# Kernel optimization log

Hardware: AMD Instinct MI355X
Metric: run time of the kernel (lower is better)

Reference implementation:

```python
import jax, jax.numpy as jnp
import numpy as np

N_NODES = 50000
N_EDGES = 1250000
IN_CH = 64
HID = 64
N_CLASSES = 10
N_GRAPHS = 128


def _xavier(key, shape):
    fan_out, fan_in = shape
    limit = np.sqrt(6.0 / (fan_in + fan_out))
    return jax.random.uniform(key, shape, jnp.float32, -limit, limit)


def setup_inputs() -> dict:
    key = jax.random.key(0)
    ks = jax.random.split(key, 12)
    x = jax.random.normal(ks[0], (N_NODES, IN_CH), jnp.float32)
    edge_index = jax.random.randint(ks[1], (2, N_EDGES), 0, N_NODES, jnp.int64)
    batch = jnp.sort(jax.random.randint(ks[2], (N_NODES,), 0, N_GRAPHS, jnp.int64))
    return {
        "x": x,
        "edge_index": edge_index,
        "batch": batch,
        # GraphConv i: lin_rel (weight+bias) applied to aggregated neighbors,
        # lin_root (no bias) applied to self features. Weights are [out, in].
        "W1_rel": _xavier(ks[3], (HID, IN_CH)), "b1": jnp.zeros((HID,), jnp.float32),
        "W1_root": _xavier(ks[4], (HID, IN_CH)),
        "W2_rel": _xavier(ks[5], (HID, HID)), "b2": jnp.zeros((HID,), jnp.float32),
        "W2_root": _xavier(ks[6], (HID, HID)),
        "W3_rel": _xavier(ks[7], (HID, HID)), "b3": jnp.zeros((HID,), jnp.float32),
        "W3_root": _xavier(ks[8], (HID, HID)),
        "W_lin": _xavier(ks[9], (N_CLASSES, HID)), "b_lin": jnp.zeros((N_CLASSES,), jnp.float32),
    }


def _graph_conv(x, src, dst, W_rel, b, W_root):
    # sum-aggregate neighbor features: gather at src, scatter-add at dst
    agg = jax.ops.segment_sum(x[src], dst, num_segments=N_NODES)  # [N, F]
    return agg @ W_rel.T + b + x @ W_root.T


def reference(x, edge_index, batch, W1_rel, b1, W1_root, W2_rel, b2, W2_root,
              W3_rel, b3, W3_root, W_lin, b_lin):
    src, dst = edge_index[0], edge_index[1]
    h = jax.nn.relu(_graph_conv(x, src, dst, W1_rel, b1, W1_root))
    h = jax.nn.relu(_graph_conv(h, src, dst, W2_rel, b2, W2_root))
    h = _graph_conv(h, src, dst, W3_rel, b3, W3_root)
    # global mean pool over graphs
    sums = jax.ops.segment_sum(h, batch, num_segments=N_GRAPHS)        # [G, HID]
    counts = jax.ops.segment_sum(jnp.ones((h.shape[0],), h.dtype), batch,
                                 num_segments=N_GRAPHS)
    pooled = sums / jnp.maximum(counts, 1.0)[:, None]
    out = pooled @ W_lin.T + b_lin  # dropout inactive in eval mode
    return (pooled, out)
```

## Files before the change

kernel.cpp:

```cpp
#include <hip/hip_runtime.h>

#define N_NODES   50000
#define HID       64
#define N_GRAPHS  128
#define N_CLASSES 10
#define NP        196
#define EPA       8192
#define PCAP      8192

typedef __attribute__((ext_vector_type(8))) short short8;
typedef __attribute__((ext_vector_type(4))) float f32x4;

__device__ __forceinline__ unsigned bf16rne(float f) {
    unsigned u = __float_as_uint(f);
    return (u + 0x7fffu + ((u >> 16) & 1u)) >> 16;
}
__device__ __forceinline__ unsigned pack_bf16x2(float lo, float hi) {
    return bf16rne(lo) | (bf16rne(hi) << 16);
}



__global__ void cvt_kernel(const float* __restrict__ x, unsigned short* __restrict__ xb,
                           int* __restrict__ gcursor, const int* __restrict__ batch,
                           int* __restrict__ gstart) {
    int i = blockIdx.x * blockDim.x + threadIdx.x;
    if (blockIdx.x == 0 && threadIdx.x < NP) gcursor[threadIdx.x] = 0;
    if (i < N_NODES) {
        int b = batch[i];
        int bp = (i > 0) ? batch[i - 1] : -1;
        for (int g = bp + 1; g <= b; ++g) gstart[g] = i;
        if (i == N_NODES - 1)
            for (int g = b + 1; g <= N_GRAPHS; ++g) gstart[g] = N_NODES;
    }
    if (i < N_NODES * 16) {
        float4 v = ((const float4*)x)[i];
        uint2 o;
        o.x = pack_bf16x2(v.x, v.y);
        o.y = pack_bf16x2(v.z, v.w);
        ((uint2*)xb)[i] = o;
    }
}


__global__ __launch_bounds__(256) void bucket_kernel(
    const int* __restrict__ src, const int* __restrict__ dst,
    int* __restrict__ gcursor, unsigned* __restrict__ packed, int E) {
    __shared__ int hist[NP], scp[NP], base[NP], cnt2[NP];
    __shared__ int sc[256];
    __shared__ unsigned stag[EPA];
    const int t = threadIdx.x;
    const int e0 = blockIdx.x * EPA;
    const int e1 = min(e0 + EPA, E);
    for (int i = t; i < NP; i += 256) { hist[i] = 0; cnt2[i] = 0; }
    __syncthreads();
    for (int e = e0 + t; e < e1; e += 256)
        atomicAdd(&hist[dst[e] >> 8], 1);
    __syncthreads();
    sc[t] = (t < NP) ? hist[t] : 0;
    __syncthreads();
    for (int off = 1; off < 256; off <<= 1) {
        int add = (t >= off) ? sc[t - off] : 0;
        __syncthreads();
        sc[t] += add;
        __syncthreads();
    }
    if (t < NP) {
        scp[t] = sc[t] - hist[t];
        if (hist[t] > 0) base[t] = atomicAdd(&gcursor[t], hist[t]);
    }
    __syncthreads();
    for (int e = e0 + t; e < e1; e += 256) {
        int d = dst[e], s = src[e];
        int p = d >> 8;
        int idx = scp[p] + atomicAdd(&cnt2[p], 1);
        stag[idx] = (unsigned)s | ((unsigned)(d & 255) << 16) | ((unsigned)p << 24);
    }
    __syncthreads();
    const int n = e1 - e0;
    for (int i = t; i < n; i += 256) {
        unsigned v = stag[i];
        int p = v >> 24;
        packed[(size_t)p * PCAP + base[p] + (i - scp[p])] = v & 0x00FFFFFFu;
    }
}

__global__ __launch_bounds__(256) void build_kernel(
    const unsigned* __restrict__ packed, const int* __restrict__ gcursor,
    int* __restrict__ offsets, unsigned short* __restrict__ csr,
    int* __restrict__ sums_zero) {
    __shared__ int hist[256], lofs[256], cnt[256], sc[256], gv[256];
    __shared__ unsigned short lcsr[PCAP];
    const int p = blockIdx.x, t = threadIdx.x;

    if (p == 0) {
        for (int i = t; i < N_GRAPHS * 64; i += 256) sums_zero[i] = 0;
    }

    int v = (t < NP) ? gcursor[t] : 0;
    sc[t] = v; gv[t] = v;
    __syncthreads();
    for (int off = 1; off < 256; off <<= 1) {
        int add = (t >= off) ? sc[t - off] : 0;
        __syncthreads();
        sc[t] += add;
        __syncthreads();
    }
    const int pb = sc[p] - gv[p];
    const int ne = gv[p];
    if (p == NP - 1 && t == 0) offsets[N_NODES] = sc[NP - 1];
    __syncthreads();

    const unsigned* mypk = packed + (size_t)p * PCAP;
    hist[t] = 0; cnt[t] = 0;
    __syncthreads();
    for (int i = t; i < ne; i += 256)
        atomicAdd(&hist[(mypk[i] >> 16) & 255], 1);
    __syncthreads();
    sc[t] = hist[t];
    __syncthreads();
    for (int off = 1; off < 256; off <<= 1) {
        int add = (t >= off) ? sc[t - off] : 0;
        __syncthreads();
        sc[t] += add;
        __syncthreads();
    }
    lofs[t] = sc[t] - hist[t];
    int node = p * 256 + t;
    if (node < N_NODES) offsets[node] = pb + lofs[t];
    __syncthreads();
    for (int i = t; i < ne; i += 256) {
        unsigned vv = mypk[i];
        int dl = (vv >> 16) & 255;
        int slot = lofs[dl] + atomicAdd(&cnt[dl], 1);
        lcsr[slot] = (unsigned short)(vv & 0xFFFFu);
    }
    __syncthreads();
    for (int i = t; i < ne; i += 256) csr[pb + i] = lcsr[i];
}


template <int RELU, int POOL>
__global__ __launch_bounds__(256) void layer_kernel(
    const unsigned short* __restrict__ hin,
    const int* __restrict__ offsets, const unsigned short* __restrict__ csr_src,
    const float* __restrict__ Wrel, const float* __restrict__ bias,
    const float* __restrict__ Wroot, unsigned short* __restrict__ hout,
    const int* __restrict__ batch, float* __restrict__ sums) {
    __shared__ short8 wfrag[2][4][2][4][16];
    __shared__ unsigned short agg_lds[32][72];

    const int tid = threadIdx.x;
    const int w = tid >> 6, lane = tid & 63;
    const int g0 = blockIdx.x * 32;

    for (int f = tid; f < 1024; f += 256) {
        int m = f >> 9;
        int r = f & 511;
        int t = r >> 7, s = (r >> 6) & 1, q = (r >> 4) & 3, c = r & 15;
        const float* W = m ? Wroot : Wrel;
        const float4* pw = (const float4*)(W + (t * 16 + c) * 64 + s * 32 + q * 8);
        float4 v0 = pw[0], v1 = pw[1];
        short8 fr;
        fr[0] = (short)bf16rne(v0.x); fr[1] = (short)bf16rne(v0.y);
        fr[2] = (short)bf16rne(v0.z); fr[3] = (short)bf16rne(v0.w);
        fr[4] = (short)bf16rne(v1.x); fr[5] = (short)bf16rne(v1.y);
        fr[6] = (short)bf16rne(v1.z); fr[7] = (short)bf16rne(v1.w);
        wfrag[m][t][s][q][c] = fr;
    }

    {
        const int rg = lane >> 3;
        const int cg = lane & 7;
        const int nb = g0 + w * 8;
        int myoff = (lane < 9) ? offsets[min(nb + lane, N_NODES)] : 0;
        for (int i = 0; i < 8; ++i) {
            const int beg = __shfl(myoff, i), end = __shfl(myoff, i + 1);
            float acc[8] = {0.f, 0.f, 0.f, 0.f, 0.f, 0.f, 0.f, 0.f};
            for (int base = beg; base < end; base += 64) {
                int cnt = min(64, end - base);
                int sidx = (base + lane < end) ? (int)csr_src[base + lane] : 0;
                for (int kb = 0; kb < cnt; kb += 32) {
                    uint4 u[4];
#pragma unroll
                    for (int p = 0; p < 4; ++p) {
                        int e = kb + 8 * p + rg;
                        int r = __shfl(sidx, e);
                        u[p] = (e < cnt) ? *((const uint4*)(hin + (size_t)r * 64) + cg)
                                         : make_uint4(0u, 0u, 0u, 0u);
                    }
#pragma unroll
                    for (int p = 0; p < 4; ++p) {
                        acc[0] += __uint_as_float(u[p].x << 16);
                        acc[1] += __uint_as_float(u[p].x & 0xffff0000u);
                        acc[2] += __uint_as_float(u[p].y << 16);
                        acc[3] += __uint_as_float(u[p].y & 0xffff0000u);
                        acc[4] += __uint_as_float(u[p].z << 16);
                        acc[5] += __uint_as_float(u[p].z & 0xffff0000u);
                        acc[6] += __uint_as_float(u[p].w << 16);
                        acc[7] += __uint_as_float(u[p].w & 0xffff0000u);
                    }
                }
            }
#pragma unroll
            for (int m = 8; m <= 32; m <<= 1)
#pragma unroll
                for (int j = 0; j < 8; ++j)
                    acc[j] += __shfl_xor(acc[j], m);
            if (rg == 0) {
                uint4 o;
                o.x = pack_bf16x2(acc[0], acc[1]);
                o.y = pack_bf16x2(acc[2], acc[3]);
                o.z = pack_bf16x2(acc[4], acc[5]);
                o.w = pack_bf16x2(acc[6], acc[7]);
                *((uint4*)&agg_lds[w * 8 + i][cg * 8]) = o;
            }
        }
    }

    __syncthreads();

    const int ng = w >> 1;
    const int th = w & 1;
    const int q = lane >> 4, c = lane & 15;
    const int n0 = g0 + ng * 16;

    short8 a_agg[2], a_x[2];
#pragma unroll
    for (int s = 0; s < 2; ++s) {
        a_agg[s] = *(const short8*)&agg_lds[ng * 16 + c][s * 32 + q * 8];
        a_x[s]   = *(const short8*)(hin + (size_t)min(n0 + c, N_NODES - 1) * 64 + s * 32 + q * 8);
    }

    f32x4 acc4[2];
#pragma unroll
    for (int tt = 0; tt < 2; ++tt) {
        const int t = th * 2 + tt;
        float bv = bias[t * 16 + c];
        f32x4 a0 = {bv, bv, bv, bv};
        a0 = __builtin_amdgcn_mfma_f32_16x16x32_bf16(a_agg[0], wfrag[0][t][0][q][c], a0, 0, 0, 0);
        a0 = __builtin_amdgcn_mfma_f32_16x16x32_bf16(a_agg[1], wfrag[0][t][1][q][c], a0, 0, 0, 0);
        a0 = __builtin_amdgcn_mfma_f32_16x16x32_bf16(a_x[0],   wfrag[1][t][0][q][c], a0, 0, 0, 0);
        a0 = __builtin_amdgcn_mfma_f32_16x16x32_bf16(a_x[1],   wfrag[1][t][1][q][c], a0, 0, 0, 0);
        acc4[tt] = a0;
    }

    if (POOL) {
        int nlast = n0 + 15;
        int b0 = batch[min(n0, N_NODES - 1)];
        int b15 = (nlast < N_NODES) ? batch[nlast] : -1;
        if (b0 == b15) {
#pragma unroll
            for (int tt = 0; tt < 2; ++tt) {
                const int t = th * 2 + tt;
                float s = acc4[tt][0] + acc4[tt][1] + acc4[tt][2] + acc4[tt][3];
                s += __shfl_xor(s, 16);
                s += __shfl_xor(s, 32);
                if (q == 0) atomicAdd(&sums[b0 * 64 + t * 16 + c], s);
            }
        } else {
#pragma unroll
            for (int r = 0; r < 4; ++r) {
                int n = n0 + q * 4 + r;
                if (n < N_NODES) {
                    int bq = batch[n];
#pragma unroll
                    for (int tt = 0; tt < 2; ++tt)
                        atomicAdd(&sums[bq * 64 + (th * 2 + tt) * 16 + c], acc4[tt][r]);
                }
            }
        }
    } else {
        __syncthreads();
#pragma unroll
        for (int tt = 0; tt < 2; ++tt) {
            const int t = th * 2 + tt;
#pragma unroll
            for (int r = 0; r < 4; ++r) {
                float v = acc4[tt][r];
                if (RELU) v = fmaxf(v, 0.f);
                agg_lds[ng * 16 + q * 4 + r][t * 16 + c] = (unsigned short)bf16rne(v);
            }
        }
        __syncthreads();
        {
            int row = w * 8 + (lane >> 3);
            int ch = (lane & 7) * 8;
            int n = g0 + row;
            if (n < N_NODES) {
                short8 v = *(const short8*)&agg_lds[row][ch];
                *(short8*)(hout + (size_t)n * 64 + ch) = v;
            }
        }
    }
}


__global__ void final_kernel(const float* __restrict__ sums, const int* __restrict__ gstart,
                             const float* __restrict__ Wlin, const float* __restrict__ blin,
                             float* __restrict__ out) {
    __shared__ float pl[64];
    int g = blockIdx.x, lane = threadIdx.x;
    float cdiv = fmaxf((float)(gstart[g + 1] - gstart[g]), 1.0f);
    float p = sums[g * 64 + lane] / cdiv;
    out[g * 64 + lane] = p;
    pl[lane] = p;
    __syncthreads();
    if (lane < N_CLASSES) {
        float o = blin[lane];
#pragma unroll
        for (int k = 0; k < 64; ++k) o += pl[k] * Wlin[lane * 64 + k];
        out[N_GRAPHS * 64 + g * N_CLASSES + lane] = o;
    }
}


extern "C" void kernel_launch(void* const* d_in, const int* in_sizes, int n_in,
                              void* d_out, int out_size, void* d_ws, size_t ws_size,
                              hipStream_t stream) {
    const float* x     = (const float*)d_in[0];
    const int*   ei    = (const int*)d_in[1];
    const int*   batch = (const int*)d_in[2];
    const float* W1r = (const float*)d_in[3];
    const float* b1  = (const float*)d_in[4];
    const float* W1o = (const float*)d_in[5];
    const float* W2r = (const float*)d_in[6];
    const float* b2  = (const float*)d_in[7];
    const float* W2o = (const float*)d_in[8];
    const float* W3r = (const float*)d_in[9];
    const float* b3  = (const float*)d_in[10];
    const float* W3o = (const float*)d_in[11];
    const float* Wl  = (const float*)d_in[12];
    const float* bl  = (const float*)d_in[13];
    float* out = (float*)d_out;

    const int E = in_sizes[1] / 2;
    const int* src = ei;
    const int* dst = ei + E;

    char* p = (char*)d_ws;
    unsigned short* xb  = (unsigned short*)p; p += (size_t)N_NODES * 64 * 2;
    unsigned short* h1  = (unsigned short*)p; p += (size_t)N_NODES * 64 * 2;
    unsigned short* h2  = (unsigned short*)p; p += (size_t)N_NODES * 64 * 2;
    unsigned* packed    = (unsigned*)p; p += (size_t)NP * PCAP * 4;
    unsigned short* csr = (unsigned short*)p; p += (size_t)E * 2;
    int* offsets   = (int*)p;   p += (size_t)(N_NODES + 1) * 4;
    int* gcursor   = (int*)p;   p += NP * 4;
    float* sums    = (float*)p; p += (size_t)N_GRAPHS * 64 * 4;
    int* gstart    = (int*)p;   p += (N_GRAPHS + 1) * 4;

    const int NCHUNK = (E + EPA - 1) / EPA;
    cvt_kernel<<<(N_NODES * 16 + 255) / 256, 256, 0, stream>>>(x, xb, gcursor, batch, gstart);
    bucket_kernel<<<NCHUNK, 256, 0, stream>>>(src, dst, gcursor, packed, E);
    build_kernel<<<NP, 256, 0, stream>>>(packed, gcursor, offsets, csr, (int*)sums);

    const int LB = (N_NODES + 31) / 32;
    layer_kernel<1, 0><<<LB, 256, 0, stream>>>(xb, offsets, csr, W1r, b1, W1o, h1, batch, sums);
    layer_kernel<1, 0><<<LB, 256, 0, stream>>>(h1, offsets, csr, W2r, b2, W2o, h2, batch, sums);
    layer_kernel<0, 1><<<LB, 256, 0, stream>>>(h2, offsets, csr, W3r, b3, W3o, h1, batch, sums);

    final_kernel<<<N_GRAPHS, 64, 0, stream>>>(sums, gstart, Wl, bl, out);
}
```

Baseline: 234.2 us.

## Split node features into two channel-half planes and gather each half separately

Node features in bf16 are now stored as two planes of 32 channels each (64 bytes per node) in place of one interleaved 128-byte row. The aggregation gathers neighbours one plane at a time, with 8-byte loads per lane and half as many accumulators. The aim is to shrink the working set of each gather pass so it fits better in cache, and to cut register pressure. The cost is walking the edge list twice and issuing twice as many smaller, less efficient gather loads.

```diff
diff --git a/kernel.cpp b/kernel.cpp
--- a/kernel.cpp
+++ b/kernel.cpp
@@ -7,6 +7,7 @@
 #define NP        196
 #define EPA       8192
 #define PCAP      8192
+#define NS32      ((size_t)N_NODES * 32)
 
 typedef __attribute__((ext_vector_type(8))) short short8;
 typedef __attribute__((ext_vector_type(4))) float f32x4;
@@ -38,7 +39,9 @@
         uint2 o;
         o.x = pack_bf16x2(v.x, v.y);
         o.y = pack_bf16x2(v.z, v.w);
-        ((uint2*)xb)[i] = o;
+        int node = i >> 4, grp = i & 15;
+        int s = grp >> 3;
+        *((uint2*)(xb + (size_t)s * NS32 + (size_t)node * 32) + (grp & 7)) = o;
     }
 }
 
@@ -174,46 +177,44 @@
         const int cg = lane & 7;
         const int nb = g0 + w * 8;
         int myoff = (lane < 9) ? offsets[min(nb + lane, N_NODES)] : 0;
-        for (int i = 0; i < 8; ++i) {
-            const int beg = __shfl(myoff, i), end = __shfl(myoff, i + 1);
-            float acc[8] = {0.f, 0.f, 0.f, 0.f, 0.f, 0.f, 0.f, 0.f};
-            for (int base = beg; base < end; base += 64) {
-                int cnt = min(64, end - base);
-                int sidx = (base + lane < end) ? (int)csr_src[base + lane] : 0;
-                for (int kb = 0; kb < cnt; kb += 32) {
-                    uint4 u[4];
-#pragma unroll
-                    for (int p = 0; p < 4; ++p) {
-                        int e = kb + 8 * p + rg;
-                        int r = __shfl(sidx, e);
-                        u[p] = (e < cnt) ? *((const uint4*)(hin + (size_t)r * 64) + cg)
-                                         : make_uint4(0u, 0u, 0u, 0u);
-                    }
-#pragma unroll
-                    for (int p = 0; p < 4; ++p) {
-                        acc[0] += __uint_as_float(u[p].x << 16);
-                        acc[1] += __uint_as_float(u[p].x & 0xffff0000u);
-                        acc[2] += __uint_as_float(u[p].y << 16);
-                        acc[3] += __uint_as_float(u[p].y & 0xffff0000u);
-                        acc[4] += __uint_as_float(u[p].z << 16);
-                        acc[5] += __uint_as_float(u[p].z & 0xffff0000u);
-                        acc[6] += __uint_as_float(u[p].w << 16);
-                        acc[7] += __uint_as_float(u[p].w & 0xffff0000u);
+#pragma unroll
+        for (int sl = 0; sl < 2; ++sl) {
+            const unsigned short* hsl = hin + (size_t)sl * NS32;
+            for (int i = 0; i < 8; ++i) {
+                const int beg = __shfl(myoff, i), end = __shfl(myoff, i + 1);
+                float acc[4] = {0.f, 0.f, 0.f, 0.f};
+                for (int base = beg; base < end; base += 64) {
+                    int cnt = min(64, end - base);
+                    int sidx = (base + lane < end) ? (int)csr_src[base + lane] : 0;
+                    for (int kb = 0; kb < cnt; kb += 32) {
+                        uint2 u[4];
+#pragma unroll
+                        for (int p = 0; p < 4; ++p) {
+                            int e = kb + 8 * p + rg;
+                            int r = __shfl(sidx, e);
+                            u[p] = (e < cnt) ? *((const uint2*)(hsl + (size_t)r * 32) + cg)
+                                             : make_uint2(0u, 0u);
+                        }
+#pragma unroll
+                        for (int p = 0; p < 4; ++p) {
+                            acc[0] += __uint_as_float(u[p].x << 16);
+                            acc[1] += __uint_as_float(u[p].x & 0xffff0000u);
+                            acc[2] += __uint_as_float(u[p].y << 16);
+                            acc[3] += __uint_as_float(u[p].y & 0xffff0000u);
+                        }
                     }
                 }
-            }
-#pragma unroll
-            for (int m = 8; m <= 32; m <<= 1)
-#pragma unroll
-                for (int j = 0; j < 8; ++j)
-                    acc[j] += __shfl_xor(acc[j], m);
-            if (rg == 0) {
-                uint4 o;
-                o.x = pack_bf16x2(acc[0], acc[1]);
-                o.y = pack_bf16x2(acc[2], acc[3]);
-                o.z = pack_bf16x2(acc[4], acc[5]);
-                o.w = pack_bf16x2(acc[6], acc[7]);
-                *((uint4*)&agg_lds[w * 8 + i][cg * 8]) = o;
+#pragma unroll
+                for (int m = 8; m <= 32; m <<= 1)
+#pragma unroll
+                    for (int j = 0; j < 4; ++j)
+                        acc[j] += __shfl_xor(acc[j], m);
+                if (rg == 0) {
+                    uint2 o;
+                    o.x = pack_bf16x2(acc[0], acc[1]);
+                    o.y = pack_bf16x2(acc[2], acc[3]);
+                    *((uint2*)&agg_lds[w * 8 + i][sl * 32 + cg * 4]) = o;
+                }
             }
         }
     }
@@ -229,7 +230,8 @@
 #pragma unroll
     for (int s = 0; s < 2; ++s) {
         a_agg[s] = *(const short8*)&agg_lds[ng * 16 + c][s * 32 + q * 8];
-        a_x[s]   = *(const short8*)(hin + (size_t)min(n0 + c, N_NODES - 1) * 64 + s * 32 + q * 8);
+        a_x[s]   = *(const short8*)(hin + (size_t)s * NS32
+                       + (size_t)min(n0 + c, N_NODES - 1) * 32 + q * 8);
     }
 
     f32x4 acc4[2];
@@ -286,10 +288,11 @@
         {
             int row = w * 8 + (lane >> 3);
             int ch = (lane & 7) * 8;
+            int s = ch >> 5;
             int n = g0 + row;
             if (n < N_NODES) {
                 short8 v = *(const short8*)&agg_lds[row][ch];
-                *(short8*)(hout + (size_t)n * 64 + ch) = v;
+                *(short8*)(hout + (size_t)s * NS32 + (size_t)n * 32 + (ch & 31)) = v;
             }
         }
     }
```

Result: slower. 251.4 us (+7.3%).

## Software-pipeline neighbor gathers across nodes with double-buffered loads; halve EPA

Applied to the files above, without the earlier changes.

Restructures the per-warp neighbor aggregation so that all eight nodes' CSR indices are loaded up front. The first 32-edge gather for the next node is issued before the current node is consumed, using two alternating register buffers. This aims to hide global gather latency behind the accumulate and reduction work, at the cost of more registers and possibly lower occupancy. It also halves the EPA constant, which changes a work-partition size in another phase.

```diff
diff --git a/kernel.cpp b/kernel.cpp
--- a/kernel.cpp
+++ b/kernel.cpp
@@ -5,7 +5,7 @@
 #define N_GRAPHS  128
 #define N_CLASSES 10
 #define NP        196
-#define EPA       8192
+#define EPA       4096
 #define PCAP      8192
 
 typedef __attribute__((ext_vector_type(8))) short short8;
@@ -174,48 +174,102 @@
         const int cg = lane & 7;
         const int nb = g0 + w * 8;
         int myoff = (lane < 9) ? offsets[min(nb + lane, N_NODES)] : 0;
+        int begs[8], cnts[8], sidx[8];
+#pragma unroll
         for (int i = 0; i < 8; ++i) {
-            const int beg = __shfl(myoff, i), end = __shfl(myoff, i + 1);
-            float acc[8] = {0.f, 0.f, 0.f, 0.f, 0.f, 0.f, 0.f, 0.f};
-            for (int base = beg; base < end; base += 64) {
-                int cnt = min(64, end - base);
-                int sidx = (base + lane < end) ? (int)csr_src[base + lane] : 0;
-                for (int kb = 0; kb < cnt; kb += 32) {
-                    uint4 u[4];
-#pragma unroll
-                    for (int p = 0; p < 4; ++p) {
-                        int e = kb + 8 * p + rg;
-                        int r = __shfl(sidx, e);
-                        u[p] = (e < cnt) ? *((const uint4*)(hin + (size_t)r * 64) + cg)
-                                         : make_uint4(0u, 0u, 0u, 0u);
-                    }
-#pragma unroll
-                    for (int p = 0; p < 4; ++p) {
-                        acc[0] += __uint_as_float(u[p].x << 16);
-                        acc[1] += __uint_as_float(u[p].x & 0xffff0000u);
-                        acc[2] += __uint_as_float(u[p].y << 16);
-                        acc[3] += __uint_as_float(u[p].y & 0xffff0000u);
-                        acc[4] += __uint_as_float(u[p].z << 16);
-                        acc[5] += __uint_as_float(u[p].z & 0xffff0000u);
-                        acc[6] += __uint_as_float(u[p].w << 16);
-                        acc[7] += __uint_as_float(u[p].w & 0xffff0000u);
-                    }
-                }
-            }
-#pragma unroll
-            for (int m = 8; m <= 32; m <<= 1)
-#pragma unroll
-                for (int j = 0; j < 8; ++j)
-                    acc[j] += __shfl_xor(acc[j], m);
-            if (rg == 0) {
-                uint4 o;
-                o.x = pack_bf16x2(acc[0], acc[1]);
-                o.y = pack_bf16x2(acc[2], acc[3]);
-                o.z = pack_bf16x2(acc[4], acc[5]);
-                o.w = pack_bf16x2(acc[6], acc[7]);
-                *((uint4*)&agg_lds[w * 8 + i][cg * 8]) = o;
-            }
-        }
+            int beg = __shfl(myoff, i), end = __shfl(myoff, i + 1);
+            begs[i] = beg; cnts[i] = end - beg;
+            sidx[i] = (beg + lane < end) ? (int)csr_src[beg + lane] : 0;
+        }
+
+        uint4 bA[4], bB[4];
+#define LOADN(i, buf)                                                         \
+        {                                                                     \
+            _Pragma("unroll")                                                 \
+            for (int p = 0; p < 4; ++p) {                                     \
+                int e = 8 * p + rg;                                           \
+                int r = __shfl(sidx[i], e);                                   \
+                buf[p] = (e < cnts[i])                                        \
+                    ? *((const uint4*)(hin + (size_t)r * 64) + cg)            \
+                    : make_uint4(0u, 0u, 0u, 0u);                             \
+            }                                                                 \
+        }
+#define UNPACK(buf, acc)                                                      \
+        {                                                                     \
+            _Pragma("unroll")                                                 \
+            for (int p = 0; p < 4; ++p) {                                     \
+                acc[0] += __uint_as_float(buf[p].x << 16);                    \
+                acc[1] += __uint_as_float(buf[p].x & 0xffff0000u);            \
+                acc[2] += __uint_as_float(buf[p].y << 16);                    \
+                acc[3] += __uint_as_float(buf[p].y & 0xffff0000u);            \
+                acc[4] += __uint_as_float(buf[p].z << 16);                    \
+                acc[5] += __uint_as_float(buf[p].z & 0xffff0000u);            \
+                acc[6] += __uint_as_float(buf[p].w << 16);                    \
+                acc[7] += __uint_as_float(buf[p].w & 0xffff0000u);            \
+            }                                                                 \
+        }
+#define CONSUME(i, buf)                                                       \
+        {                                                                     \
+            float acc[8] = {0.f,0.f,0.f,0.f,0.f,0.f,0.f,0.f};                 \
+            UNPACK(buf, acc);                                                 \
+            if (cnts[i] > 32) {               \
+                uint4 u2[4];                                                  \
+                _Pragma("unroll")                                             \
+                for (int p = 0; p < 4; ++p) {                                 \
+                    int e = 32 + 8 * p + rg;                                  \
+                    int r = __shfl(sidx[i], e);                               \
+                    u2[p] = (e < cnts[i])                                     \
+                        ? *((const uint4*)(hin + (size_t)r * 64) + cg)        \
+                        : make_uint4(0u, 0u, 0u, 0u);                         \
+                }                                                             \
+                UNPACK(u2, acc);                                              \
+            }                                                                 \
+            if (cnts[i] > 64) {                 \
+                int end = begs[i] + cnts[i];                                  \
+                for (int base = begs[i] + 64; base < end; base += 64) {       \
+                    int cnt = min(64, end - base);                            \
+                    int sid = (base + lane < end) ? (int)csr_src[base + lane] : 0; \
+                    for (int kb = 0; kb < cnt; kb += 32) {                    \
+                        uint4 u3[4];                                          \
+                        _Pragma("unroll")                                     \
+                        for (int p = 0; p < 4; ++p) {                         \
+                            int e = kb + 8 * p + rg;                          \
+                            int r = __shfl(sid, e);                           \
+                            u3[p] = (e < cnt)                                 \
+                                ? *((const uint4*)(hin + (size_t)r * 64) + cg) \
+                                : make_uint4(0u, 0u, 0u, 0u);                 \
+                        }                                                     \
+                        UNPACK(u3, acc);                                      \
+                    }                                                         \
+                }                                                             \
+            }                                                                 \
+            _Pragma("unroll")                                                 \
+            for (int m = 8; m <= 32; m <<= 1)                                 \
+                _Pragma("unroll")                                             \
+                for (int j = 0; j < 8; ++j)                                   \
+                    acc[j] += __shfl_xor(acc[j], m);                          \
+            if (rg == 0) {                                                    \
+                uint4 o;                                                      \
+                o.x = pack_bf16x2(acc[0], acc[1]);                            \
+                o.y = pack_bf16x2(acc[2], acc[3]);                            \
+                o.z = pack_bf16x2(acc[4], acc[5]);                            \
+                o.w = pack_bf16x2(acc[6], acc[7]);                            \
+                *((uint4*)&agg_lds[w * 8 + (i)][cg * 8]) = o;                 \
+            }                                                                 \
+        }
+
+        LOADN(0, bA); LOADN(1, bB);
+        CONSUME(0, bA); LOADN(2, bA);
+        CONSUME(1, bB); LOADN(3, bB);
+        CONSUME(2, bA); LOADN(4, bA);
+        CONSUME(3, bB); LOADN(5, bB);
+        CONSUME(4, bA); LOADN(6, bA);
+        CONSUME(5, bB); LOADN(7, bB);
+        CONSUME(6, bA);
+        CONSUME(7, bB);
+#undef LOADN
+#undef UNPACK
+#undef CONSUME
     }
 
     __syncthreads();
```

Result: no change. 234.8 us (+0.2%).

## Fuse all stages into one cooperative persistent kernel with grid syncs

Applied to the files above, without the earlier changes.

Replaces the seven separate launches (convert, bucket, build, three layers, final) with a single cooperative persistent kernel. Work is distributed over virtual blocks in grid-stride loops, and grid.sync() separates the stages. The intent is to remove per-launch overhead and the inter-kernel gaps, and the edge chunk size is halved to raise parallelism in the bucket phase. The cost is grid-wide barriers, a capped resident grid that may lower occupancy in the layer phases, and a non-inlined layer function.

```diff
diff --git a/kernel.cpp b/kernel.cpp
--- a/kernel.cpp
+++ b/kernel.cpp
@@ -1,12 +1,17 @@
 #include <hip/hip_runtime.h>
+#include <hip/hip_cooperative_groups.h>
+
+namespace cg = cooperative_groups;
 
 #define N_NODES   50000
 #define HID       64
 #define N_GRAPHS  128
 #define N_CLASSES 10
 #define NP        196
-#define EPA       8192
+#define EPA       4096
 #define PCAP      8192
+#define NCVT      3125
+#define NVL       1563
 
 typedef __attribute__((ext_vector_type(8))) short short8;
 typedef __attribute__((ext_vector_type(4))) float f32x4;
@@ -19,144 +24,29 @@
     return bf16rne(lo) | (bf16rne(hi) << 16);
 }
 
-
-
-__global__ void cvt_kernel(const float* __restrict__ x, unsigned short* __restrict__ xb,
-                           int* __restrict__ gcursor, const int* __restrict__ batch,
-                           int* __restrict__ gstart) {
-    int i = blockIdx.x * blockDim.x + threadIdx.x;
-    if (blockIdx.x == 0 && threadIdx.x < NP) gcursor[threadIdx.x] = 0;
-    if (i < N_NODES) {
-        int b = batch[i];
-        int bp = (i > 0) ? batch[i - 1] : -1;
-        for (int g = bp + 1; g <= b; ++g) gstart[g] = i;
-        if (i == N_NODES - 1)
-            for (int g = b + 1; g <= N_GRAPHS; ++g) gstart[g] = N_NODES;
-    }
-    if (i < N_NODES * 16) {
-        float4 v = ((const float4*)x)[i];
-        uint2 o;
-        o.x = pack_bf16x2(v.x, v.y);
-        o.y = pack_bf16x2(v.z, v.w);
-        ((uint2*)xb)[i] = o;
-    }
-}
-
-
-__global__ __launch_bounds__(256) void bucket_kernel(
-    const int* __restrict__ src, const int* __restrict__ dst,
-    int* __restrict__ gcursor, unsigned* __restrict__ packed, int E) {
-    __shared__ int hist[NP], scp[NP], base[NP], cnt2[NP];
-    __shared__ int sc[256];
-    __shared__ unsigned stag[EPA];
-    const int t = threadIdx.x;
-    const int e0 = blockIdx.x * EPA;
-    const int e1 = min(e0 + EPA, E);
-    for (int i = t; i < NP; i += 256) { hist[i] = 0; cnt2[i] = 0; }
-    __syncthreads();
-    for (int e = e0 + t; e < e1; e += 256)
-        atomicAdd(&hist[dst[e] >> 8], 1);
-    __syncthreads();
-    sc[t] = (t < NP) ? hist[t] : 0;
-    __syncthreads();
-    for (int off = 1; off < 256; off <<= 1) {
-        int add = (t >= off) ? sc[t - off] : 0;
-        __syncthreads();
-        sc[t] += add;
-        __syncthreads();
-    }
-    if (t < NP) {
-        scp[t] = sc[t] - hist[t];
-        if (hist[t] > 0) base[t] = atomicAdd(&gcursor[t], hist[t]);
-    }
-    __syncthreads();
-    for (int e = e0 + t; e < e1; e += 256) {
-        int d = dst[e], s = src[e];
-        int p = d >> 8;
-        int idx = scp[p] + atomicAdd(&cnt2[p], 1);
-        stag[idx] = (unsigned)s | ((unsigned)(d & 255) << 16) | ((unsigned)p << 24);
-    }
-    __syncthreads();
-    const int n = e1 - e0;
-    for (int i = t; i < n; i += 256) {
-        unsigned v = stag[i];
-        int p = v >> 24;
-        packed[(size_t)p * PCAP + base[p] + (i - scp[p])] = v & 0x00FFFFFFu;
-    }
-}
-
-__global__ __launch_bounds__(256) void build_kernel(
-    const unsigned* __restrict__ packed, const int* __restrict__ gcursor,
-    int* __restrict__ offsets, unsigned short* __restrict__ csr,
-    int* __restrict__ sums_zero) {
-    __shared__ int hist[256], lofs[256], cnt[256], sc[256], gv[256];
-    __shared__ unsigned short lcsr[PCAP];
-    const int p = blockIdx.x, t = threadIdx.x;
-
-    if (p == 0) {
-        for (int i = t; i < N_GRAPHS * 64; i += 256) sums_zero[i] = 0;
-    }
-
-    int v = (t < NP) ? gcursor[t] : 0;
-    sc[t] = v; gv[t] = v;
-    __syncthreads();
-    for (int off = 1; off < 256; off <<= 1) {
-        int add = (t >= off) ? sc[t - off] : 0;
-        __syncthreads();
-        sc[t] += add;
-        __syncthreads();
-    }
-    const int pb = sc[p] - gv[p];
-    const int ne = gv[p];
-    if (p == NP - 1 && t == 0) offsets[N_NODES] = sc[NP - 1];
-    __syncthreads();
-
-    const unsigned* mypk = packed + (size_t)p * PCAP;
-    hist[t] = 0; cnt[t] = 0;
-    __syncthreads();
-    for (int i = t; i < ne; i += 256)
-        atomicAdd(&hist[(mypk[i] >> 16) & 255], 1);
-    __syncthreads();
-    sc[t] = hist[t];
-    __syncthreads();
-    for (int off = 1; off < 256; off <<= 1) {
-        int add = (t >= off) ? sc[t - off] : 0;
-        __syncthreads();
-        sc[t] += add;
-        __syncthreads();
-    }
-    lofs[t] = sc[t] - hist[t];
-    int node = p * 256 + t;
-    if (node < N_NODES) offsets[node] = pb + lofs[t];
-    __syncthreads();
-    for (int i = t; i < ne; i += 256) {
-        unsigned vv = mypk[i];
-        int dl = (vv >> 16) & 255;
-        int slot = lofs[dl] + atomicAdd(&cnt[dl], 1);
-        lcsr[slot] = (unsigned short)(vv & 0xFFFFu);
-    }
-    __syncthreads();
-    for (int i = t; i < ne; i += 256) csr[pb + i] = lcsr[i];
-}
-
-
-template <int RELU, int POOL>
-__global__ __launch_bounds__(256) void layer_kernel(
-    const unsigned short* __restrict__ hin,
-    const int* __restrict__ offsets, const unsigned short* __restrict__ csr_src,
-    const float* __restrict__ Wrel, const float* __restrict__ bias,
-    const float* __restrict__ Wroot, unsigned short* __restrict__ hout,
-    const int* __restrict__ batch, float* __restrict__ sums) {
-    __shared__ short8 wfrag[2][4][2][4][16];
-    __shared__ unsigned short agg_lds[32][72];
-
+struct MegaArgs {
+    const float* x; const int* src; const int* dst; const int* batch;
+    const float* W1r; const float* b1; const float* W1o;
+    const float* W2r; const float* b2; const float* W2o;
+    const float* W3r; const float* b3; const float* W3o;
+    const float* Wl; const float* bl;
+    unsigned short* xb; unsigned short* h1; unsigned short* h2;
+    unsigned* packed; unsigned short* csr; int* offsets; int* gcursor;
+    float* sums; int* gstart; float* out; int E; int nchunk;
+};
+
+__device__ __noinline__ void layer_phase(char* smem,
+    const unsigned short* hin, const int* offsets, const unsigned short* csr_src,
+    const float* Wrel, const float* bias, const float* Wroot,
+    unsigned short* hout, const int* batch, float* sums,
+    int relu, int pool) {
+    short8* wfrag = (short8*)smem;
+    unsigned short (*agg_lds)[72] = (unsigned short (*)[72])(smem + 16384);
     const int tid = threadIdx.x;
     const int w = tid >> 6, lane = tid & 63;
-    const int g0 = blockIdx.x * 32;
 
     for (int f = tid; f < 1024; f += 256) {
-        int m = f >> 9;
-        int r = f & 511;
+        int m = f >> 9, r = f & 511;
         int t = r >> 7, s = (r >> 6) & 1, q = (r >> 4) & 3, c = r & 15;
         const float* W = m ? Wroot : Wrel;
         const float4* pw = (const float4*)(W + (t * 16 + c) * 64 + s * 32 + q * 8);
@@ -166,124 +56,127 @@
         fr[2] = (short)bf16rne(v0.z); fr[3] = (short)bf16rne(v0.w);
         fr[4] = (short)bf16rne(v1.x); fr[5] = (short)bf16rne(v1.y);
         fr[6] = (short)bf16rne(v1.z); fr[7] = (short)bf16rne(v1.w);
-        wfrag[m][t][s][q][c] = fr;
-    }
-
-    {
-        const int rg = lane >> 3;
-        const int cg = lane & 7;
-        const int nb = g0 + w * 8;
-        int myoff = (lane < 9) ? offsets[min(nb + lane, N_NODES)] : 0;
-        for (int i = 0; i < 8; ++i) {
-            const int beg = __shfl(myoff, i), end = __shfl(myoff, i + 1);
-            float acc[8] = {0.f, 0.f, 0.f, 0.f, 0.f, 0.f, 0.f, 0.f};
-            for (int base = beg; base < end; base += 64) {
-                int cnt = min(64, end - base);
-                int sidx = (base + lane < end) ? (int)csr_src[base + lane] : 0;
-                for (int kb = 0; kb < cnt; kb += 32) {
-                    uint4 u[4];
-#pragma unroll
-                    for (int p = 0; p < 4; ++p) {
-                        int e = kb + 8 * p + rg;
-                        int r = __shfl(sidx, e);
-                        u[p] = (e < cnt) ? *((const uint4*)(hin + (size_t)r * 64) + cg)
-                                         : make_uint4(0u, 0u, 0u, 0u);
+        wfrag[(((m * 4 + t) * 2 + s) * 4 + q) * 16 + c] = fr;
+    }
+
+    for (int vb = blockIdx.x; vb < NVL; vb += gridDim.x) {
+        __syncthreads();
+        const int g0 = vb * 32;
+
+        {
+            const int rg = lane >> 3;
+            const int cg = lane & 7;
+            const int nb = g0 + w * 8;
+            int myoff = (lane < 9) ? offsets[min(nb + lane, N_NODES)] : 0;
+            for (int i = 0; i < 8; ++i) {
+                const int beg = __shfl(myoff, i), end = __shfl(myoff, i + 1);
+                float acc[8] = {0.f, 0.f, 0.f, 0.f, 0.f, 0.f, 0.f, 0.f};
+                for (int base = beg; base < end; base += 64) {
+                    int cnt = min(64, end - base);
+                    int sidx = (base + lane < end) ? (int)csr_src[base + lane] : 0;
+                    for (int kb = 0; kb < cnt; kb += 32) {
+                        uint4 u[4];
+#pragma unroll
+                        for (int p = 0; p < 4; ++p) {
+                            int e = kb + 8 * p + rg;
+                            int r = __shfl(sidx, e);
+                            u[p] = (e < cnt) ? *((const uint4*)(hin + (size_t)r * 64) + cg)
+                                             : make_uint4(0u, 0u, 0u, 0u);
+                        }
+#pragma unroll
+                        for (int p = 0; p < 4; ++p) {
+                            acc[0] += __uint_as_float(u[p].x << 16);
+                            acc[1] += __uint_as_float(u[p].x & 0xffff0000u);
+                            acc[2] += __uint_as_float(u[p].y << 16);
+                            acc[3] += __uint_as_float(u[p].y & 0xffff0000u);
+                            acc[4] += __uint_as_float(u[p].z << 16);
+                            acc[5] += __uint_as_float(u[p].z & 0xffff0000u);
+                            acc[6] += __uint_as_float(u[p].w << 16);
+                            acc[7] += __uint_as_float(u[p].w & 0xffff0000u);
+                        }
                     }
-#pragma unroll
-                    for (int p = 0; p < 4; ++p) {
-                        acc[0] += __uint_as_float(u[p].x << 16);
-                        acc[1] += __uint_as_float(u[p].x & 0xffff0000u);
-                        acc[2] += __uint_as_float(u[p].y << 16);
-                        acc[3] += __uint_as_float(u[p].y & 0xffff0000u);
-                        acc[4] += __uint_as_float(u[p].z << 16);
-                        acc[5] += __uint_as_float(u[p].z & 0xffff0000u);
-                        acc[6] += __uint_as_float(u[p].w << 16);
-                        acc[7] += __uint_as_float(u[p].w & 0xffff0000u);
+                }
+#pragma unroll
+                for (int m = 8; m <= 32; m <<= 1)
+#pragma unroll
+                    for (int j = 0; j < 8; ++j)
+                        acc[j] += __shfl_xor(acc[j], m);
+                if (rg == 0) {
+                    uint4 o;
+                    o.x = pack_bf16x2(acc[0], acc[1]);
+                    o.y = pack_bf16x2(acc[2], acc[3]);
+                    o.z = pack_bf16x2(acc[4], acc[5]);
+                    o.w = pack_bf16x2(acc[6], acc[7]);
+                    *((uint4*)&agg_lds[w * 8 + i][cg * 8]) = o;
+                }
+            }
+        }
+
+        __syncthreads();
+
+        const int ng = w >> 1;
+        const int th = w & 1;
+        const int q = lane >> 4, c = lane & 15;
+        const int n0 = g0 + ng * 16;
+
+        short8 a_agg[2], a_x[2];
+#pragma unroll
+        for (int s = 0; s < 2; ++s) {
+            a_agg[s] = *(const short8*)&agg_lds[ng * 16 + c][s * 32 + q * 8];
+            a_x[s]   = *(const short8*)(hin + (size_t)min(n0 + c, N_NODES - 1) * 64 + s * 32 + q * 8);
+        }
+
+        f32x4 acc4[2];
+#pragma unroll
+        for (int tt = 0; tt < 2; ++tt) {
+            const int t = th * 2 + tt;
+            float bv = bias[t * 16 + c];
+            f32x4 a0 = {bv, bv, bv, bv};
+            a0 = __builtin_amdgcn_mfma_f32_16x16x32_bf16(a_agg[0], wfrag[(((0*4+t)*2+0)*4+q)*16+c], a0, 0, 0, 0);
+            a0 = __builtin_amdgcn_mfma_f32_16x16x32_bf16(a_agg[1], wfrag[(((0*4+t)*2+1)*4+q)*16+c], a0, 0, 0, 0);
+            a0 = __builtin_amdgcn_mfma_f32_16x16x32_bf16(a_x[0],   wfrag[(((1*4+t)*2+0)*4+q)*16+c], a0, 0, 0, 0);
+            a0 = __builtin_amdgcn_mfma_f32_16x16x32_bf16(a_x[1],   wfrag[(((1*4+t)*2+1)*4+q)*16+c], a0, 0, 0, 0);
+            acc4[tt] = a0;
+        }
+
+        if (pool) {
+            int nlast = n0 + 15;
+            int b0 = batch[min(n0, N_NODES - 1)];
+            int b15 = (nlast < N_NODES) ? batch[nlast] : -1;
+            if (b0 == b15) {
+#pragma unroll
+                for (int tt = 0; tt < 2; ++tt) {
+                    const int t = th * 2 + tt;
+                    float s = acc4[tt][0] + acc4[tt][1] + acc4[tt][2] + acc4[tt][3];
+                    s += __shfl_xor(s, 16);
+                    s += __shfl_xor(s, 32);
+                    if (q == 0) atomicAdd(&sums[b0 * 64 + t * 16 + c], s);
+                }
+            } else {
+#pragma unroll
+                for (int r = 0; r < 4; ++r) {
+                    int n = n0 + q * 4 + r;
+                    if (n < N_NODES) {
+                        int bq = batch[n];
+#pragma unroll
+                        for (int tt = 0; tt < 2; ++tt)
+                            atomicAdd(&sums[bq * 64 + (th * 2 + tt) * 16 + c], acc4[tt][r]);
                     }
                 }
             }
-#pragma unroll
-            for (int m = 8; m <= 32; m <<= 1)
-#pragma unroll
-                for (int j = 0; j < 8; ++j)
-                    acc[j] += __shfl_xor(acc[j], m);
-            if (rg == 0) {
-                uint4 o;
-                o.x = pack_bf16x2(acc[0], acc[1]);
-                o.y = pack_bf16x2(acc[2], acc[3]);
-                o.z = pack_bf16x2(acc[4], acc[5]);
-                o.w = pack_bf16x2(acc[6], acc[7]);
-                *((uint4*)&agg_lds[w * 8 + i][cg * 8]) = o;
-            }
-        }
-    }
-
-    __syncthreads();
-
-    const int ng = w >> 1;
-    const int th = w & 1;
-    const int q = lane >> 4, c = lane & 15;
-    const int n0 = g0 + ng * 16;
-
-    short8 a_agg[2], a_x[2];
-#pragma unroll
-    for (int s = 0; s < 2; ++s) {
-        a_agg[s] = *(const short8*)&agg_lds[ng * 16 + c][s * 32 + q * 8];
-        a_x[s]   = *(const short8*)(hin + (size_t)min(n0 + c, N_NODES - 1) * 64 + s * 32 + q * 8);
-    }
-
-    f32x4 acc4[2];
-#pragma unroll
-    for (int tt = 0; tt < 2; ++tt) {
-        const int t = th * 2 + tt;
-        float bv = bias[t * 16 + c];
-        f32x4 a0 = {bv, bv, bv, bv};
-        a0 = __builtin_amdgcn_mfma_f32_16x16x32_bf16(a_agg[0], wfrag[0][t][0][q][c], a0, 0, 0, 0);
-        a0 = __builtin_amdgcn_mfma_f32_16x16x32_bf16(a_agg[1], wfrag[0][t][1][q][c], a0, 0, 0, 0);
-        a0 = __builtin_amdgcn_mfma_f32_16x16x32_bf16(a_x[0],   wfrag[1][t][0][q][c], a0, 0, 0, 0);
-        a0 = __builtin_amdgcn_mfma_f32_16x16x32_bf16(a_x[1],   wfrag[1][t][1][q][c], a0, 0, 0, 0);
-        acc4[tt] = a0;
-    }
-
-    if (POOL) {
-        int nlast = n0 + 15;
-        int b0 = batch[min(n0, N_NODES - 1)];
-        int b15 = (nlast < N_NODES) ? batch[nlast] : -1;
-        if (b0 == b15) {
+        } else {
+            __syncthreads();
 #pragma unroll
             for (int tt = 0; tt < 2; ++tt) {
                 const int t = th * 2 + tt;
-                float s = acc4[tt][0] + acc4[tt][1] + acc4[tt][2] + acc4[tt][3];
-                s += __shfl_xor(s, 16);
-                s += __shfl_xor(s, 32);
-                if (q == 0) atomicAdd(&sums[b0 * 64 + t * 16 + c], s);
-            }
-        } else {
-#pragma unroll
-            for (int r = 0; r < 4; ++r) {
-                int n = n0 + q * 4 + r;
-                if (n < N_NODES) {
-                    int bq = batch[n];
-#pragma unroll
-                    for (int tt = 0; tt < 2; ++tt)
-                        atomicAdd(&sums[bq * 64 + (th * 2 + tt) * 16 + c], acc4[tt][r]);
-                }
-            }
-        }
-    } else {
-        __syncthreads();
-#pragma unroll
-        for (int tt = 0; tt < 2; ++tt) {
-            const int t = th * 2 + tt;
-#pragma unroll
-            for (int r = 0; r < 4; ++r) {
-                float v = acc4[tt][r];
-                if (RELU) v = fmaxf(v, 0.f);
-                agg_lds[ng * 16 + q * 4 + r][t * 16 + c] = (unsigned short)bf16rne(v);
-            }
-        }
-        __syncthreads();
-        {
+#pragma unroll
+                for (int r = 0; r < 4; ++r) {
+                    float v = acc4[tt][r];
+                    if (relu) v = fmaxf(v, 0.f);
+                    agg_lds[ng * 16 + q * 4 + r][t * 16 + c] = (unsigned short)bf16rne(v);
+                }
+            }
+            __syncthreads();
             int row = w * 8 + (lane >> 3);
             int ch = (lane & 7) * 8;
             int n = g0 + row;
@@ -295,22 +188,164 @@
     }
 }
 
-
-__global__ void final_kernel(const float* __restrict__ sums, const int* __restrict__ gstart,
-                             const float* __restrict__ Wlin, const float* __restrict__ blin,
-                             float* __restrict__ out) {
-    __shared__ float pl[64];
-    int g = blockIdx.x, lane = threadIdx.x;
-    float cdiv = fmaxf((float)(gstart[g + 1] - gstart[g]), 1.0f);
-    float p = sums[g * 64 + lane] / cdiv;
-    out[g * 64 + lane] = p;
-    pl[lane] = p;
-    __syncthreads();
-    if (lane < N_CLASSES) {
-        float o = blin[lane];
-#pragma unroll
-        for (int k = 0; k < 64; ++k) o += pl[k] * Wlin[lane * 64 + k];
-        out[N_GRAPHS * 64 + g * N_CLASSES + lane] = o;
+__global__ void __launch_bounds__(256) mega_kernel(MegaArgs a) {
+    __shared__ __align__(16) char smem[21504];
+    cg::grid_group grid = cg::this_grid();
+    const int tid = threadIdx.x;
+    const int bid = blockIdx.x;
+    const int gsz = gridDim.x;
+
+    if (bid == 0 && tid < NP) a.gcursor[tid] = 0;
+    __threadfence();
+    grid.sync();
+
+    {
+        const int NC = a.nchunk;
+        for (int vb = bid; vb < NC + NCVT + NP; vb += gsz) {
+            if (vb < NC) {
+                int* hist  = (int*)smem;
+                int* scp   = (int*)(smem + 1024);
+                int* basep = (int*)(smem + 2048);
+                int* cnt2  = (int*)(smem + 3072);
+                int* sc    = (int*)(smem + 4096);
+                unsigned* stag = (unsigned*)(smem + 5120);
+                const int e0 = vb * EPA;
+                const int e1 = min(e0 + EPA, a.E);
+                __syncthreads();
+                for (int i = tid; i < NP; i += 256) { hist[i] = 0; cnt2[i] = 0; }
+                __syncthreads();
+                for (int e = e0 + tid; e < e1; e += 256)
+                    atomicAdd(&hist[a.dst[e] >> 8], 1);
+                __syncthreads();
+                sc[tid] = (tid < NP) ? hist[tid] : 0;
+                __syncthreads();
+                for (int off = 1; off < 256; off <<= 1) {
+                    int add = (tid >= off) ? sc[tid - off] : 0;
+                    __syncthreads();
+                    sc[tid] += add;
+                    __syncthreads();
+                }
+                if (tid < NP) {
+                    scp[tid] = sc[tid] - hist[tid];
+                    if (hist[tid] > 0) basep[tid] = atomicAdd(&a.gcursor[tid], hist[tid]);
+                }
+                __syncthreads();
+                for (int e = e0 + tid; e < e1; e += 256) {
+                    int d = a.dst[e], s = a.src[e];
+                    int pp = d >> 8;
+                    int idx = scp[pp] + atomicAdd(&cnt2[pp], 1);
+                    stag[idx] = (unsigned)s | ((unsigned)(d & 255) << 16) | ((unsigned)pp << 24);
+                }
+                __syncthreads();
+                const int n = e1 - e0;
+                for (int i = tid; i < n; i += 256) {
+                    unsigned v = stag[i];
+                    int pp = v >> 24;
+                    a.packed[(size_t)pp * PCAP + basep[pp] + (i - scp[pp])] = v & 0x00FFFFFFu;
+                }
+            } else if (vb < NC + NCVT) {
+                int u = vb - NC;
+                if (u < 32) a.sums[u * 256 + tid] = 0.f;
+                int i = u * 256 + tid;
+                if (i < N_NODES * 16) {
+                    float4 v = ((const float4*)a.x)[i];
+                    uint2 o;
+                    o.x = pack_bf16x2(v.x, v.y);
+                    o.y = pack_bf16x2(v.z, v.w);
+                    ((uint2*)a.xb)[i] = o;
+                }
+            } else {
+                int v = vb - NC - NCVT;
+                int node = v * 256 + tid;
+                if (node < N_NODES) {
+                    int b = a.batch[node];
+                    int bp = (node > 0) ? a.batch[node - 1] : -1;
+                    for (int g = bp + 1; g <= b; ++g) a.gstart[g] = node;
+                    if (node == N_NODES - 1)
+                        for (int g = b + 1; g <= N_GRAPHS; ++g) a.gstart[g] = N_NODES;
+                }
+            }
+        }
+    }
+    __threadfence();
+    grid.sync();
+
+    for (int vb = bid; vb < NP; vb += gsz) {
+        int* hist = (int*)smem;
+        int* lofs = (int*)(smem + 1024);
+        int* cnt  = (int*)(smem + 2048);
+        int* sc   = (int*)(smem + 3072);
+        int* gv   = (int*)(smem + 4096);
+        unsigned short* lcsr = (unsigned short*)(smem + 5120);
+        const int p = vb;
+        __syncthreads();
+        int v = (tid < NP) ? a.gcursor[tid] : 0;
+        sc[tid] = v; gv[tid] = v;
+        __syncthreads();
+        for (int off = 1; off < 256; off <<= 1) {
+            int add = (tid >= off) ? sc[tid - off] : 0;
+            __syncthreads();
+            sc[tid] += add;
+            __syncthreads();
+        }
+        const int pb = sc[p] - gv[p];
+        const int ne = gv[p];
+        if (p == NP - 1 && tid == 0) a.offsets[N_NODES] = sc[NP - 1];
+        __syncthreads();
+        const unsigned* mypk = a.packed + (size_t)p * PCAP;
+        hist[tid] = 0; cnt[tid] = 0;
+        __syncthreads();
+        for (int i = tid; i < ne; i += 256)
+            atomicAdd(&hist[(mypk[i] >> 16) & 255], 1);
+        __syncthreads();
+        sc[tid] = hist[tid];
+        __syncthreads();
+        for (int off = 1; off < 256; off <<= 1) {
+            int add = (tid >= off) ? sc[tid - off] : 0;
+            __syncthreads();
+            sc[tid] += add;
+            __syncthreads();
+        }
+        lofs[tid] = sc[tid] - hist[tid];
+        int node = p * 256 + tid;
+        if (node < N_NODES) a.offsets[node] = pb + lofs[tid];
+        __syncthreads();
+        for (int i = tid; i < ne; i += 256) {
+            unsigned vv = mypk[i];
+            int dl = (vv >> 16) & 255;
+            int slot = lofs[dl] + atomicAdd(&cnt[dl], 1);
+            lcsr[slot] = (unsigned short)(vv & 0xFFFFu);
+        }
+        __syncthreads();
+        for (int i = tid; i < ne; i += 256) a.csr[pb + i] = lcsr[i];
+        __syncthreads();
+    }
+    __threadfence();
+    grid.sync();
+
+    layer_phase(smem, a.xb, a.offsets, a.csr, a.W1r, a.b1, a.W1o, a.h1, a.batch, a.sums, 1, 0);
+    __threadfence();
+    grid.sync();
+    layer_phase(smem, a.h1, a.offsets, a.csr, a.W2r, a.b2, a.W2o, a.h2, a.batch, a.sums, 1, 0);
+    __threadfence();
+    grid.sync();
+    layer_phase(smem, a.h2, a.offsets, a.csr, a.W3r, a.b3, a.W3o, a.h1, a.batch, a.sums, 0, 1);
+    __threadfence();
+    grid.sync();
+
+    for (int vb = bid; vb < N_GRAPHS / 4; vb += gsz) {
+        const int w = tid >> 6, lane = tid & 63;
+        int g = vb * 4 + w;
+        float cdiv = fmaxf((float)(a.gstart[g + 1] - a.gstart[g]), 1.0f);
+        float pv = a.sums[g * 64 + lane] / cdiv;
+        a.out[g * 64 + lane] = pv;
+        float o = (lane < N_CLASSES) ? a.bl[lane] : 0.f;
+#pragma unroll
+        for (int k = 0; k < 64; ++k) {
+            float pk = __shfl(pv, k);
+            if (lane < N_CLASSES) o += pk * a.Wl[lane * 64 + k];
+        }
+        if (lane < N_CLASSES) a.out[N_GRAPHS * 64 + g * N_CLASSES + lane] = o;
     }
 }
 
@@ -321,22 +356,8 @@
     const float* x     = (const float*)d_in[0];
     const int*   ei    = (const int*)d_in[1];
     const int*   batch = (const int*)d_in[2];
-    const float* W1r = (const float*)d_in[3];
-    const float* b1  = (const float*)d_in[4];
-    const float* W1o = (const float*)d_in[5];
-    const float* W2r = (const float*)d_in[6];
-    const float* b2  = (const float*)d_in[7];
-    const float* W2o = (const float*)d_in[8];
-    const float* W3r = (const float*)d_in[9];
-    const float* b3  = (const float*)d_in[10];
-    const float* W3o = (const float*)d_in[11];
-    const float* Wl  = (const float*)d_in[12];
-    const float* bl  = (const float*)d_in[13];
-    float* out = (float*)d_out;
 
     const int E = in_sizes[1] / 2;
-    const int* src = ei;
-    const int* dst = ei + E;
 
     char* p = (char*)d_ws;
     unsigned short* xb  = (unsigned short*)p; p += (size_t)N_NODES * 64 * 2;
@@ -349,15 +370,23 @@
     float* sums    = (float*)p; p += (size_t)N_GRAPHS * 64 * 4;
     int* gstart    = (int*)p;   p += (N_GRAPHS + 1) * 4;
 
-    const int NCHUNK = (E + EPA - 1) / EPA;
-    cvt_kernel<<<(N_NODES * 16 + 255) / 256, 256, 0, stream>>>(x, xb, gcursor, batch, gstart);
-    bucket_kernel<<<NCHUNK, 256, 0, stream>>>(src, dst, gcursor, packed, E);
-    build_kernel<<<NP, 256, 0, stream>>>(packed, gcursor, offsets, csr, (int*)sums);
-
-    const int LB = (N_NODES + 31) / 32;
-    layer_kernel<1, 0><<<LB, 256, 0, stream>>>(xb, offsets, csr, W1r, b1, W1o, h1, batch, sums);
-    layer_kernel<1, 0><<<LB, 256, 0, stream>>>(h1, offsets, csr, W2r, b2, W2o, h2, batch, sums);
-    layer_kernel<0, 1><<<LB, 256, 0, stream>>>(h2, offsets, csr, W3r, b3, W3o, h1, batch, sums);
-
-    final_kernel<<<N_GRAPHS, 64, 0, stream>>>(sums, gstart, Wl, bl, out);
-}
+    MegaArgs ha;
+    ha.x = x; ha.src = ei; ha.dst = ei + E; ha.batch = batch;
+    ha.W1r = (const float*)d_in[3];  ha.b1 = (const float*)d_in[4];  ha.W1o = (const float*)d_in[5];
+    ha.W2r = (const float*)d_in[6];  ha.b2 = (const float*)d_in[7];  ha.W2o = (const float*)d_in[8];
+    ha.W3r = (const float*)d_in[9];  ha.b3 = (const float*)d_in[10]; ha.W3o = (const float*)d_in[11];
+    ha.Wl  = (const float*)d_in[12]; ha.bl = (const float*)d_in[13];
+    ha.xb = xb; ha.h1 = h1; ha.h2 = h2;
+    ha.packed = packed; ha.csr = csr; ha.offsets = offsets; ha.gcursor = gcursor;
+    ha.sums = sums; ha.gstart = gstart; ha.out = (float*)d_out;
+    ha.E = E; ha.nchunk = (E + EPA - 1) / EPA;
+
+    int nb = 0;
+    hipOccupancyMaxActiveBlocksPerMultiprocessor(&nb, mega_kernel, 256, 0);
+    if (nb < 1) nb = 1;
+    int grid = nb * 256;
+    if (grid > 1568) grid = 1568;
+
+    void* args[] = { (void*)&ha };
+    hipLaunchCooperativeKernel(mega_kernel, dim3(grid), dim3(256), args, 0, stream);
+}
```

Result: slower. 908.3 us (+287.8%).
